# Performance work log

Measured on AMD Instinct MI355X. Metric: run time of the kernel, lower is better.

## Reference

```python
import jax, jax.numpy as jnp
import numpy as np

B, N, C = 8, 4096, 512
H, DK, DV = 8, 64, 64


def _xnorm(x, gamma):
    # L2 norm over last dim, keepdim; scale by per-head gamma
    nrm = jnp.sqrt(jnp.sum(x * x, axis=-1, keepdims=True))
    return x * gamma / nrm


def setup_inputs() -> dict:
    key = jax.random.key(0)
    ks = jax.random.split(key, 9)
    inp = {
        "queries": jax.random.normal(ks[0], (B, N, C), dtype=jnp.float32),
        "keys": jax.random.normal(ks[1], (B, N, C), dtype=jnp.float32),
        "values": jax.random.normal(ks[2], (B, N, C), dtype=jnp.float32),
        # Linear weights stored torch-style [out, in]; init.normal_(std=0.001), bias=0
        "Wq": jax.random.normal(ks[3], (H * DK, C), dtype=jnp.float32) * 0.001,
        "bq": jnp.zeros((H * DK,), dtype=jnp.float32),
        "Wk": jax.random.normal(ks[4], (H * DK, C), dtype=jnp.float32) * 0.001,
        "bk": jnp.zeros((H * DK,), dtype=jnp.float32),
        "Wv": jax.random.normal(ks[5], (H * DV, C), dtype=jnp.float32) * 0.001,
        "bv": jnp.zeros((H * DV,), dtype=jnp.float32),
        "Wo": jax.random.normal(ks[6], (C, H * DV), dtype=jnp.float32) * 0.001,
        "bo": jnp.zeros((C,), dtype=jnp.float32),
        "gamma": jax.random.normal(ks[7], (1, H, 1, 1), dtype=jnp.float32),
    }
    return inp


def reference(queries, keys, values, Wq, bq, Wk, bk, Wv, bv, Wo, bo, gamma):
    bs, nq, _ = queries.shape
    nk = keys.shape[1]
    # projections -> [b, h, n, d]
    q = (queries @ Wq.T + bq).reshape(bs, nq, H, DK).transpose(0, 2, 1, 3)
    k = (keys @ Wk.T + bk).reshape(bs, nk, H, DK).transpose(0, 2, 1, 3)
    v = (values @ Wv.T + bv).reshape(bs, nk, H, DV).transpose(0, 2, 1, 3)
    # kv: [b, h, dk, dv]  (small intermediate)
    kv = jnp.einsum('bhnk,bhnv->bhkv', k, v)
    kv_n = _xnorm(kv, gamma)     # norm over dv
    q_n = _xnorm(q, gamma)       # norm over dk
    out = jnp.einsum('bhnk,bhkv->bhnv', q_n, kv_n)  # [b,h,nq,dv]
    out = out.transpose(0, 2, 1, 3).reshape(bs, nq, H * DV)
    return out @ Wo.T + bo
```

## Files before the change

### kernel.cpp

```cpp
#include <hip/hip_runtime.h>


typedef __attribute__((ext_vector_type(4))) float f32x4;
typedef __attribute__((ext_vector_type(8))) short s16x8;
typedef __attribute__((ext_vector_type(4))) unsigned short u16x4;
typedef __attribute__((ext_vector_type(8))) unsigned short u16x8;
typedef __attribute__((ext_vector_type(2))) unsigned u32x2;

#define DEVFN __device__ __forceinline__

DEVFN unsigned short f2b(float f) {
  union { float f; unsigned u; } un; un.f = f;
  unsigned r = un.u + 0x7fffu + ((un.u >> 16) & 1u);
  return (unsigned short)(r >> 16);
}
DEVFN float b2f(unsigned short us) {
  union { unsigned u; float f; } un; un.u = ((unsigned)us) << 16;
  return un.f;
}
DEVFN unsigned pk2(float x0, float x1) {
  union { float f; unsigned u; } a, b;
  a.f = x0; b.f = x1;
  return __builtin_amdgcn_perm(b.u + 0x8000u, a.u + 0x8000u, 0x07060302u);
}
DEVFN void gl_lds16(const void* g, void* l) {
  __builtin_amdgcn_global_load_lds(
      (const __attribute__((address_space(1))) unsigned*)g,
      (__attribute__((address_space(3))) unsigned*)l, 16, 0, 0);
}

template <bool AF32, typename CT>
DEVFN void gemmN512(const void* Ain, const unsigned short* Bt,
                    const float* bias, CT* C, bool qnorm,
                    const float* gamma, int bx) {
  __shared__ __align__(16) char LA[2][8192];
  __shared__ __align__(16) char LB[2][32768];
  const int tid = threadIdx.x, lane = tid & 63, wid = tid >> 6;
  const int r = lane & 15, g = lane >> 4;
  const int mw = wid >> 3;
  const int nw = wid & 7;

  const char* BsS = (const char*)Bt + (long)(wid * 32 + (lane >> 2)) * 1024 +
                    (((lane & 3) ^ ((lane >> 3) & 3)) * 16);

  const char* AfS = nullptr;
  const char* AsS = nullptr;
  int awr = 0;
  if constexpr (AF32) {
    AfS = (const char*)Ain + (long)(bx * 128 + (tid >> 3)) * 2048 +
          (tid & 7) * 16;
    const int row = tid >> 3, p = tid & 7;
    awr = row * 64 + (((p >> 1) ^ ((row >> 1) & 3)) << 4) + (p & 1) * 8;
  } else {
    AsS = (const char*)Ain + (long)(bx * 128 + wid * 16 + (lane >> 2)) * 1024 +
          (((lane & 3) ^ ((lane >> 3) & 3)) * 16);
  }

  f32x4 acc[4][4] = {};
  f32x4 pa;

#define SGB(BUF, KT)                                                           \
  gl_lds16(BsS + (KT)*64, LB[BUF] + wid * 2048);                               \
  gl_lds16(BsS + 16384 + (KT)*64, LB[BUF] + wid * 2048 + 1024);
#define SGA(BUF, KT)                                                           \
  if (wid < 8) { gl_lds16(AsS + (KT)*64, LA[BUF] + wid * 1024); }
#define LDA(KT) pa = *reinterpret_cast<const f32x4*>(AfS + (KT)*128);
#define WRA(BUF)                                                               \
  {                                                                            \
    u32x2 w;                                                                   \
    w[0] = pk2(pa[0], pa[1]);                                                  \
    w[1] = pk2(pa[2], pa[3]);                                                  \
    *reinterpret_cast<u32x2*>(LA[BUF] + awr) = w;                              \
  }
#define COMPUTE(BUF)                                                           \
  {                                                                            \
    s16x8 a[4], b[4];                                                          \
    _Pragma("unroll") for (int i = 0; i < 4; ++i) {                            \
      int ar = mw * 64 + i * 16 + r;                                           \
      a[i] = *reinterpret_cast<const s16x8*>(                                  \
          LA[BUF] + ar * 64 + ((g ^ ((ar >> 1) & 3)) << 4));                   \
    }                                                                          \
    _Pragma("unroll") for (int j = 0; j < 4; ++j) {                            \
      int br = nw * 64 + j * 16 + r;                                           \
      b[j] = *reinterpret_cast<const s16x8*>(                                  \
          LB[BUF] + br * 64 + ((g ^ ((br >> 1) & 3)) << 4));                   \
    }                                                                          \
    _Pragma("unroll") for (int i = 0; i < 4; ++i)                              \
        _Pragma("unroll") for (int j = 0; j < 4; ++j) acc[i][j] =              \
        __builtin_amdgcn_mfma_f32_16x16x32_bf16(a[i], b[j], acc[i][j], 0, 0,   \
                                                0);                            \
  }

  if constexpr (AF32) {
    LDA(0) WRA(0)
  } else {
    SGA(0, 0)
  }
  SGB(0, 0)
  __syncthreads();

#pragma unroll 1
  for (int t = 0; t < 15; ++t) {
    const int cur = t & 1, nxt = cur ^ 1;
    if constexpr (AF32) { LDA(t + 1) }
    SGB(nxt, t + 1)
    if constexpr (!AF32) { SGA(nxt, t + 1) }
    COMPUTE(cur)
    if constexpr (AF32) { WRA(nxt) }
    __syncthreads();
  }
  COMPUTE(1)

#undef SGB
#undef SGA
#undef LDA
#undef WRA
#undef COMPUTE

  const int crow0 = bx * 128 + mw * 64 + g * 4;
  const int ccol0 = nw * 64 + r;
#pragma unroll
  for (int j = 0; j < 4; ++j) {
    float bv = bias[ccol0 + j * 16];
#pragma unroll
    for (int i = 0; i < 4; ++i)
#pragma unroll
      for (int ii = 0; ii < 4; ++ii) acc[i][j][ii] += bv;
  }
  if (qnorm) {
    const float gam = gamma[nw];
#pragma unroll
    for (int i = 0; i < 4; ++i)
#pragma unroll
      for (int ii = 0; ii < 4; ++ii) {
        float s = 0.f;
#pragma unroll
        for (int j = 0; j < 4; ++j) s += acc[i][j][ii] * acc[i][j][ii];
        s += __shfl_xor(s, 1);
        s += __shfl_xor(s, 2);
        s += __shfl_xor(s, 4);
        s += __shfl_xor(s, 8);
        float sc = gam / sqrtf(s);
#pragma unroll
        for (int j = 0; j < 4; ++j) acc[i][j][ii] *= sc;
      }
  }
#pragma unroll
  for (int i = 0; i < 4; ++i)
#pragma unroll
    for (int j = 0; j < 4; ++j)
#pragma unroll
      for (int ii = 0; ii < 4; ++ii) {
        long row = crow0 + i * 16 + ii;
        int col = ccol0 + j * 16;
        if constexpr (sizeof(CT) == 2)
          C[row * 512 + col] = f2b(acc[i][j][ii]);
        else
          C[row * 512 + col] = acc[i][j][ii];
      }
}

__global__ __launch_bounds__(1024)
void proj_qkv(const float* __restrict__ Aq, const float* __restrict__ Ak,
              const float* __restrict__ Av, const unsigned short* __restrict__ Bq,
              const unsigned short* __restrict__ Bk, const unsigned short* __restrict__ Bv,
              const float* __restrict__ bq, const float* __restrict__ bk,
              const float* __restrict__ bv, unsigned short* __restrict__ Cq,
              unsigned short* __restrict__ Ck, unsigned short* __restrict__ Cv,
              const float* __restrict__ gamma) {
  const int z = blockIdx.y;
  const float* A = z == 0 ? Aq : (z == 1 ? Ak : Av);
  const unsigned short* B = z == 0 ? Bq : (z == 1 ? Bk : Bv);
  const float* bias = z == 0 ? bq : (z == 1 ? bk : bv);
  unsigned short* C = z == 0 ? Cq : (z == 1 ? Ck : Cv);
  gemmN512<true, unsigned short>(A, B, bias, C, z == 0, gamma, blockIdx.x);
}

__global__ __launch_bounds__(1024)
void gemm_final(const unsigned short* __restrict__ q, const unsigned short* __restrict__ Mt,
                const float* __restrict__ bo, float* __restrict__ out) {
  const int zb = blockIdx.y;
  gemmN512<false, float>(q + (long)zb * 2097152, Mt + (long)zb * 262144, bo,
                         out + (long)zb * 2097152, false, nullptr, blockIdx.x);
}

#define NCHUNK 8
__global__ __launch_bounds__(256, 2)
void kv_partial(const unsigned short* __restrict__ kq,
                const unsigned short* __restrict__ vq,
                float* __restrict__ part) {
  const int tid = threadIdx.x;
  const int chunk = blockIdx.x;
  const int bh = blockIdx.y;
  const int b = bh >> 3, h = bh & 7;
  __shared__ float ks[32][64];
  __shared__ float vs[32][64];
  const int dk0 = (tid & 15) * 4;
  const int dv0 = (tid >> 4) * 4;
  float acc[4][4] = {};
  const long nbase = (long)b * 4096 + chunk * 512;
  const int lrow = tid >> 3, lc8 = tid & 7;

  for (int sub = 0; sub < 16; ++sub) {
    long n0 = nbase + sub * 32;
    {
      long gofs = (n0 + lrow) * 512 + h * 64 + lc8 * 8;
      u16x8 kk = *reinterpret_cast<const u16x8*>(kq + gofs);
      u16x8 vv = *reinterpret_cast<const u16x8*>(vq + gofs);
      f32x4 k0 = {b2f(kk[0]), b2f(kk[1]), b2f(kk[2]), b2f(kk[3])};
      f32x4 k1 = {b2f(kk[4]), b2f(kk[5]), b2f(kk[6]), b2f(kk[7])};
      f32x4 v0 = {b2f(vv[0]), b2f(vv[1]), b2f(vv[2]), b2f(vv[3])};
      f32x4 v1 = {b2f(vv[4]), b2f(vv[5]), b2f(vv[6]), b2f(vv[7])};
      *reinterpret_cast<f32x4*>(&ks[lrow][lc8 * 8]) = k0;
      *reinterpret_cast<f32x4*>(&ks[lrow][lc8 * 8 + 4]) = k1;
      *reinterpret_cast<f32x4*>(&vs[lrow][lc8 * 8]) = v0;
      *reinterpret_cast<f32x4*>(&vs[lrow][lc8 * 8 + 4]) = v1;
    }
    __syncthreads();
#pragma unroll 4
    for (int n = 0; n < 32; ++n) {
      f32x4 kk = *reinterpret_cast<const f32x4*>(&ks[n][dk0]);
      f32x4 vv = *reinterpret_cast<const f32x4*>(&vs[n][dv0]);
#pragma unroll
      for (int a = 0; a < 4; ++a)
#pragma unroll
        for (int c = 0; c < 4; ++c)
          acc[a][c] += kk[a] * vv[c];
    }
    __syncthreads();
  }
  float* pg = part + ((long)chunk * 64 + bh) * 4096;
#pragma unroll
  for (int a = 0; a < 4; ++a) {
    f32x4 o = {acc[a][0], acc[a][1], acc[a][2], acc[a][3]};
    *reinterpret_cast<f32x4*>(pg + (dk0 + a) * 64 + dv0) = o;
  }
}

__global__ __launch_bounds__(256)
void kv_norm_mt(const float* __restrict__ part, const float* __restrict__ gamma,
                const unsigned short* __restrict__ Wo_b,
                unsigned short* __restrict__ Mt) {
  const int bh = blockIdx.x, h = bh & 7, b = bh >> 3;
  const int tid = threadIdx.x;
  __shared__ float kvs[4096];
  __shared__ float scale_s[64];
  __shared__ __align__(16) unsigned short kvn_l[64 * 72];

#pragma unroll
  for (int i = 0; i < 4; ++i) {
    int e4 = i * 256 + tid;
    const float* p = part + (long)bh * 4096 + e4 * 4;
    f32x4 s = {0.f, 0.f, 0.f, 0.f};
#pragma unroll
    for (int c = 0; c < NCHUNK; ++c) {
      f32x4 v = *reinterpret_cast<const f32x4*>(p + (long)c * 64 * 4096);
      s += v;
    }
    *reinterpret_cast<f32x4*>(kvs + e4 * 4) = s;
  }
  __syncthreads();
  if (tid < 64) {
    float s = 0.f;
    for (int dv = 0; dv < 64; ++dv) { float x = kvs[tid * 64 + dv]; s += x * x; }
    scale_s[tid] = gamma[h] / sqrtf(s);
  }
  __syncthreads();
#pragma unroll
  for (int i = 0; i < 4; ++i) {
    int e4 = i * 256 + tid;
    int row = e4 >> 4, c0 = (e4 & 15) * 4;
    float sc = scale_s[row];
    f32x4 v = *reinterpret_cast<const f32x4*>(kvs + e4 * 4);
    u16x4 o = {f2b(v[0] * sc), f2b(v[1] * sc), f2b(v[2] * sc), f2b(v[3] * sc)};
    *reinterpret_cast<u16x4*>(kvn_l + row * 72 + c0) = o;
  }
  __syncthreads();

  const int seg = tid >> 6;
  const int lane = tid & 63;
  const int r = lane & 15, g = lane >> 4;
  f32x4 acc[8][4] = {};
  s16x8 bf[2][4];
#pragma unroll
  for (int ks = 0; ks < 2; ++ks)
#pragma unroll
    for (int j = 0; j < 4; ++j)
      bf[ks][j] = *reinterpret_cast<const s16x8*>(
          kvn_l + (j * 16 + r) * 72 + ks * 32 + g * 8);
#pragma unroll
  for (int ks = 0; ks < 2; ++ks)
#pragma unroll
    for (int i = 0; i < 8; ++i) {
      s16x8 af = *reinterpret_cast<const s16x8*>(
          Wo_b + (long)(seg * 128 + i * 16 + r) * 512 + h * 64 + ks * 32 + g * 8);
#pragma unroll
      for (int j = 0; j < 4; ++j)
        acc[i][j] = __builtin_amdgcn_mfma_f32_16x16x32_bf16(af, bf[ks][j], acc[i][j], 0, 0, 0);
    }
#pragma unroll
  for (int i = 0; i < 8; ++i)
#pragma unroll
    for (int j = 0; j < 4; ++j)
#pragma unroll
      for (int ii = 0; ii < 4; ++ii) {
        int c = seg * 128 + i * 16 + g * 4 + ii;
        int dk = j * 16 + r;
        Mt[(long)b * 262144 + (long)c * 512 + h * 64 + dk] = f2b(acc[i][j][ii]);
      }
}

__global__ void cast4(const float* __restrict__ a0, const float* __restrict__ a1,
                      const float* __restrict__ a2, const float* __restrict__ a3,
                      unsigned short* __restrict__ o0, unsigned short* __restrict__ o1,
                      unsigned short* __restrict__ o2, unsigned short* __restrict__ o3) {
  const int y = blockIdx.y;
  const float* in = y == 0 ? a0 : (y == 1 ? a1 : (y == 2 ? a2 : a3));
  unsigned short* out = y == 0 ? o0 : (y == 1 ? o1 : (y == 2 ? o2 : o3));
  int i = blockIdx.x * 256 + threadIdx.x;
  f32x4 v = reinterpret_cast<const f32x4*>(in)[i];
  reinterpret_cast<u16x4*>(out)[i] = u16x4{f2b(v[0]), f2b(v[1]), f2b(v[2]), f2b(v[3])};
}

extern "C" void kernel_launch(void* const* d_in, const int* in_sizes, int n_in,
                              void* d_out, int out_size, void* d_ws, size_t ws_size,
                              hipStream_t stream) {
  const float* queries = (const float*)d_in[0];
  const float* keys    = (const float*)d_in[1];
  const float* values  = (const float*)d_in[2];
  const float* Wq = (const float*)d_in[3];
  const float* bq = (const float*)d_in[4];
  const float* Wk = (const float*)d_in[5];
  const float* bk = (const float*)d_in[6];
  const float* Wv = (const float*)d_in[7];
  const float* bv = (const float*)d_in[8];
  const float* Wo = (const float*)d_in[9];
  const float* bo = (const float*)d_in[10];
  const float* gamma = (const float*)d_in[11];

  unsigned short* Wq_b = (unsigned short*)d_ws;
  unsigned short* Wk_b = Wq_b + 262144;
  unsigned short* Wv_b = Wk_b + 262144;
  unsigned short* Wo_b = Wv_b + 262144;
  unsigned short* q_b  = Wo_b + 262144;
  unsigned short* kvn  = q_b + 16777216;
  float* part = (float*)(kvn + 262144);
  unsigned short* Mt = (unsigned short*)(part + 2097152);
  unsigned short* k_b = (unsigned short*)d_out;
  unsigned short* v_b = k_b + 16777216;
  float* out = (float*)d_out;

  cast4<<<dim3(256, 4), 256, 0, stream>>>(Wq, Wk, Wv, Wo, Wq_b, Wk_b, Wv_b, Wo_b);

  proj_qkv<<<dim3(256, 3), 1024, 0, stream>>>(
      queries, keys, values, Wq_b, Wk_b, Wv_b, bq, bk, bv, q_b, k_b, v_b, gamma);

  kv_partial<<<dim3(NCHUNK, 64), 256, 0, stream>>>(k_b, v_b, part);
  kv_norm_mt<<<64, 256, 0, stream>>>(part, gamma, Wo_b, Mt);

  gemm_final<<<dim3(32, 8), 1024, 0, stream>>>(q_b, Mt, bo, out);
}
```

Before: 173.5 us.

## Triple-buffer LDS in projection GEMM with fine-grained vmcnt waits

The projection GEMM moves from a double-buffered K loop with __syncthreads to a triple-buffered, fully unrolled pipeline. Global-to-LDS loads now run two tiles ahead, and each step waits with explicit s_waitcnt vmcnt/lgkmcnt counts plus a raw s_barrier instead of draining everything. The aim is to hide global load latency behind MFMA compute. In exchange, LDS use grows by half to 120KB per block, which may cut occupancy, and correctness now depends on the hand-counted vmcnt values.

```diff
diff --git a/kernel.cpp b/kernel.cpp
--- a/kernel.cpp
+++ b/kernel.cpp
@@ -33,8 +33,8 @@
 DEVFN void gemmN512(const void* Ain, const unsigned short* Bt,
                     const float* bias, CT* C, bool qnorm,
                     const float* gamma, int bx) {
-  __shared__ __align__(16) char LA[2][8192];
-  __shared__ __align__(16) char LB[2][32768];
+  __shared__ __align__(16) char LA[3][8192];
+  __shared__ __align__(16) char LB[3][32768];
   const int tid = threadIdx.x, lane = tid & 63, wid = tid >> 6;
   const int r = lane & 15, g = lane >> 4;
   const int mw = wid >> 3;
@@ -57,19 +57,24 @@
   }
 
   f32x4 acc[4][4] = {};
-  f32x4 pa;
+  f32x4 paA, paB;
+
+#define SB0 __builtin_amdgcn_sched_barrier(0);
+#define BARR SB0 __builtin_amdgcn_s_barrier(); SB0
+#define VMC(N) asm volatile("s_waitcnt vmcnt(" #N ")" ::: "memory");
+#define LGK asm volatile("s_waitcnt lgkmcnt(0)" ::: "memory");
 
 #define SGB(BUF, KT)                                                           \
   gl_lds16(BsS + (KT)*64, LB[BUF] + wid * 2048);                               \
   gl_lds16(BsS + 16384 + (KT)*64, LB[BUF] + wid * 2048 + 1024);
 #define SGA(BUF, KT)                                                           \
   if (wid < 8) { gl_lds16(AsS + (KT)*64, LA[BUF] + wid * 1024); }
-#define LDA(KT) pa = *reinterpret_cast<const f32x4*>(AfS + (KT)*128);
-#define WRA(BUF)                                                               \
+#define LDA(P, KT) P = *reinterpret_cast<const f32x4*>(AfS + (KT)*128);
+#define WRA(P, BUF)                                                            \
   {                                                                            \
     u32x2 w;                                                                   \
-    w[0] = pk2(pa[0], pa[1]);                                                  \
-    w[1] = pk2(pa[2], pa[3]);                                                  \
+    w[0] = pk2(P[0], P[1]);                                                    \
+    w[1] = pk2(P[2], P[3]);                                                    \
     *reinterpret_cast<u32x2*>(LA[BUF] + awr) = w;                              \
   }
 #define COMPUTE(BUF)                                                           \
@@ -92,30 +97,67 @@
   }
 
   if constexpr (AF32) {
-    LDA(0) WRA(0)
+    LDA(paA, 0) WRA(paA, 0)
+    SGB(0, 0)
+    LDA(paB, 1)
+    SGB(1, 1)
+    VMC(3)
   } else {
-    SGA(0, 0)
-  }
-  SGB(0, 0)
-  __syncthreads();
-
-#pragma unroll 1
-  for (int t = 0; t < 15; ++t) {
-    const int cur = t & 1, nxt = cur ^ 1;
-    if constexpr (AF32) { LDA(t + 1) }
-    SGB(nxt, t + 1)
-    if constexpr (!AF32) { SGA(nxt, t + 1) }
-    COMPUTE(cur)
-    if constexpr (AF32) { WRA(nxt) }
-    __syncthreads();
-  }
-  COMPUTE(1)
-
+    SGA(0, 0) SGB(0, 0)
+    SGA(1, 1) SGB(1, 1)
+    if (wid < 8) { VMC(3) } else { VMC(2) }
+  }
+  LGK
+  BARR
+
+#define STEP(T, PL, PW)                                                        \
+  {                                                                            \
+    if ((T) + 2 <= 15) {                                                       \
+      if constexpr (AF32) { LDA(PL, (T) + 2) }                                 \
+      else { SGA(((T) + 2) % 3, (T) + 2) }                                     \
+      SGB(((T) + 2) % 3, (T) + 2)                                              \
+    }                                                                          \
+    COMPUTE((T) % 3)                                                           \
+    if constexpr (AF32) {                                                      \
+      if ((T) + 1 <= 15) { WRA(PW, ((T) + 1) % 3) }                            \
+    }                                                                          \
+    LGK                                                                        \
+    if ((T) < 14) {                                                            \
+      if constexpr (AF32) { VMC(3) }                                           \
+      else { if (wid < 8) { VMC(3) } else { VMC(2) } }                         \
+    } else {                                                                   \
+      VMC(0)                                                                   \
+    }                                                                          \
+    BARR                                                                       \
+  }
+
+  STEP(0, paA, paB)
+  STEP(1, paB, paA)
+  STEP(2, paA, paB)
+  STEP(3, paB, paA)
+  STEP(4, paA, paB)
+  STEP(5, paB, paA)
+  STEP(6, paA, paB)
+  STEP(7, paB, paA)
+  STEP(8, paA, paB)
+  STEP(9, paB, paA)
+  STEP(10, paA, paB)
+  STEP(11, paB, paA)
+  STEP(12, paA, paB)
+  STEP(13, paB, paA)
+  STEP(14, paA, paB)
+  COMPUTE(0)
+
+#undef STEP
 #undef SGB
 #undef SGA
 #undef LDA
 #undef WRA
 #undef COMPUTE
+#undef SB0
+#undef BARR
+#undef VMC
+#undef LGK
 
   const int crow0 = bx * 128 + mw * 64 + g * 4;
   const int ccol0 = nw * 64 + r;
```

Result: no change. 176.1 us (+1.5%).

## Deepen GEMM pipeline to four LDS buffers, two k-steps per barrier

Applied to the files above, without the earlier changes.

The shared GEMM routine used by the QKV projection and the final output GEMM moves from double to quadruple LDS buffering. Each loop iteration now prefetches two k-tiles and computes two, which halves the number of __syncthreads barriers and leaves more time to hide memory latency. LDS use rises from 80KB to 160KB per block and more registers stay live for the second A prefetch. The launch bounds also gain a second argument, which further constrains register allocation.

```diff
diff --git a/kernel.cpp b/kernel.cpp
--- a/kernel.cpp
+++ b/kernel.cpp
@@ -33,8 +33,8 @@
 DEVFN void gemmN512(const void* Ain, const unsigned short* Bt,
                     const float* bias, CT* C, bool qnorm,
                     const float* gamma, int bx) {
-  __shared__ __align__(16) char LA[2][8192];
-  __shared__ __align__(16) char LB[2][32768];
+  __shared__ __align__(16) char LA[4][8192];
+  __shared__ __align__(16) char LB[4][32768];
   const int tid = threadIdx.x, lane = tid & 63, wid = tid >> 6;
   const int r = lane & 15, g = lane >> 4;
   const int mw = wid >> 3;
@@ -57,19 +57,19 @@
   }
 
   f32x4 acc[4][4] = {};
-  f32x4 pa;
+  f32x4 paA, paB;
 
 #define SGB(BUF, KT)                                                           \
   gl_lds16(BsS + (KT)*64, LB[BUF] + wid * 2048);                               \
   gl_lds16(BsS + 16384 + (KT)*64, LB[BUF] + wid * 2048 + 1024);
 #define SGA(BUF, KT)                                                           \
   if (wid < 8) { gl_lds16(AsS + (KT)*64, LA[BUF] + wid * 1024); }
-#define LDA(KT) pa = *reinterpret_cast<const f32x4*>(AfS + (KT)*128);
-#define WRA(BUF)                                                               \
+#define LDA(P, KT) P = *reinterpret_cast<const f32x4*>(AfS + (KT)*128);
+#define WRA(P, BUF)                                                            \
   {                                                                            \
     u32x2 w;                                                                   \
-    w[0] = pk2(pa[0], pa[1]);                                                  \
-    w[1] = pk2(pa[2], pa[3]);                                                  \
+    w[0] = pk2(P[0], P[1]);                                                    \
+    w[1] = pk2(P[2], P[3]);                                                    \
     *reinterpret_cast<u32x2*>(LA[BUF] + awr) = w;                              \
   }
 #define COMPUTE(BUF)                                                           \
@@ -92,24 +92,29 @@
   }
 
   if constexpr (AF32) {
-    LDA(0) WRA(0)
+    LDA(paA, 0) WRA(paA, 0)
+    LDA(paB, 1) WRA(paB, 1)
   } else {
-    SGA(0, 0)
-  }
-  SGB(0, 0)
+    SGA(0, 0) SGA(1, 1)
+  }
+  SGB(0, 0) SGB(1, 1)
   __syncthreads();
 
 #pragma unroll 1
-  for (int t = 0; t < 15; ++t) {
-    const int cur = t & 1, nxt = cur ^ 1;
-    if constexpr (AF32) { LDA(t + 1) }
-    SGB(nxt, t + 1)
-    if constexpr (!AF32) { SGA(nxt, t + 1) }
-    COMPUTE(cur)
-    if constexpr (AF32) { WRA(nxt) }
+  for (int t0 = 0; t0 < 14; t0 += 2) {
+    const int b2 = (t0 + 2) & 3, b3 = (t0 + 3) & 3;
+    if constexpr (AF32) {
+      LDA(paA, t0 + 2) LDA(paB, t0 + 3)
+    }
+    SGB(b2, t0 + 2) SGB(b3, t0 + 3)
+    if constexpr (!AF32) { SGA(b2, t0 + 2) SGA(b3, t0 + 3) }
+    COMPUTE(t0 & 3)
+    COMPUTE((t0 + 1) & 3)
+    if constexpr (AF32) { WRA(paA, b2) WRA(paB, b3) }
     __syncthreads();
   }
-  COMPUTE(1)
+  COMPUTE(2)
+  COMPUTE(3)
 
 #undef SGB
 #undef SGA
@@ -160,7 +165,7 @@
       }
 }
 
-__global__ __launch_bounds__(1024)
+__global__ __launch_bounds__(1024, 4)
 void proj_qkv(const float* __restrict__ Aq, const float* __restrict__ Ak,
               const float* __restrict__ Av, const unsigned short* __restrict__ Bq,
               const unsigned short* __restrict__ Bk, const unsigned short* __restrict__ Bv,
@@ -176,7 +181,7 @@
   gemmN512<true, unsigned short>(A, B, bias, C, z == 0, gamma, blockIdx.x);
 }
 
-__global__ __launch_bounds__(1024)
+__global__ __launch_bounds__(1024, 4)
 void gemm_final(const unsigned short* __restrict__ q, const unsigned short* __restrict__ Mt,
                 const float* __restrict__ bo, float* __restrict__ out) {
   const int zb = blockIdx.y;
```

Result: faster. 167.4 us (-3.5%).
